# Kernel tuning notes

Measured on AMD Instinct MI355X. Metric: run time of the kernel, lower is better.

The kernel has to match this reference:

```python
import jax, jax.numpy as jnp
import numpy as np

B, C, H, Wd = 4, 64, 64, 64


def setup_inputs() -> dict:
    key = jax.random.key(0)
    k1, k2, k3 = jax.random.split(key, 3)
    x = jax.random.normal(k1, (B, C, H, Wd), dtype=jnp.float32)
    W = jax.random.normal(k2, (C, C), dtype=jnp.float32) * (1.0 / np.sqrt(C))
    b = jax.random.normal(k3, (C,), dtype=jnp.float32) * 0.01
    return {"x": x, "W": W, "b": b}


def reference(x, W, b):
    Bz, Cz, Hz, Wz = x.shape
    N = Hz * Wz
    xf = x.reshape(Bz, Cz, N)                      # values [B,C,N]
    # shared 1x1 conv for queries and keys (same module instance in torch)
    qk = jnp.einsum('oc,bcn->bon', W, xf) + b[None, :, None]  # [B,C,N]
    # scores[b,n,m] = sum_c q[b,c,n] * k[b,c,m], scaled by 1/N
    scores = jnp.einsum('bcn,bcm->bnm', qk, qk) / N           # [B,N,N]
    attn = jax.nn.softmax(scores, axis=-1)                    # softmax over m
    # out[b,c,n] = sum_m values[b,c,m] * attn[b,n,m]
    out = jnp.einsum('bcm,bnm->bcn', xf, attn)
    return out.reshape(Bz, Cz, Hz, Wz)
```

## Files before the change

kernel.cpp:

```cpp
#include <hip/hip_runtime.h>
#include <hip/hip_bf16.h>

#define BATCH 4
#define NSP   4096

typedef __bf16 bf16x8v __attribute__((ext_vector_type(8)));
typedef __bf16 bf16x4v __attribute__((ext_vector_type(4)));
typedef float  floatx4 __attribute__((ext_vector_type(4)));

__global__ __launch_bounds__(256) void qk_kernel(const float* __restrict__ x,
                                                 const float* __restrict__ Wm,
                                                 const float* __restrict__ bias,
                                                 __bf16* __restrict__ qkT) {
    __shared__ __align__(16) char smem1[18432];
    __bf16* xT   = (__bf16*)smem1;
    __bf16* Wl   = (__bf16*)(smem1 + 9216);
    float*  Olds = (float*)smem1;

    const int t  = threadIdx.x;
    const int b  = blockIdx.x >> 6;
    const int n0 = (blockIdx.x & 63) << 6;

#pragma unroll
    for (int i = 0; i < 16; ++i) {
        int idx = t + 256 * i;
        int r = idx >> 6, j = idx & 63;
        xT[j * 72 + r] = (__bf16)x[(b * 64 + r) * 4096 + n0 + j];
        Wl[r * 72 + j] = (__bf16)Wm[idx];
    }
    __syncthreads();

    const int w = t >> 6, lane = t & 63, quad = lane >> 4, l16 = lane & 15;
    const bf16x8v a0 = *(const bf16x8v*)(xT + (w * 16 + l16) * 72 + quad * 8);
    const bf16x8v a1 = *(const bf16x8v*)(xT + (w * 16 + l16) * 72 + 32 + quad * 8);

    floatx4 acc[4];
#pragma unroll
    for (int ot = 0; ot < 4; ++ot) {
        acc[ot] = floatx4{0.f, 0.f, 0.f, 0.f};
        bf16x8v b0 = *(const bf16x8v*)(Wl + (ot * 16 + l16) * 72 + quad * 8);
        bf16x8v b1 = *(const bf16x8v*)(Wl + (ot * 16 + l16) * 72 + 32 + quad * 8);
        acc[ot] = __builtin_amdgcn_mfma_f32_16x16x32_bf16(a0, b0, acc[ot], 0, 0, 0);
        acc[ot] = __builtin_amdgcn_mfma_f32_16x16x32_bf16(a1, b1, acc[ot], 0, 0, 0);
    }
    __syncthreads();

#pragma unroll
    for (int ot = 0; ot < 4; ++ot) {
        const float bo = bias[ot * 16 + l16];
#pragma unroll
        for (int r = 0; r < 4; ++r)
            Olds[(w * 16 + quad * 4 + r) * 68 + ot * 16 + l16] = acc[ot][r] + bo;
    }
    __syncthreads();

    const int n = t >> 2, seg = t & 3;
#pragma unroll
    for (int i = 0; i < 2; ++i) {
        bf16x8v pk;
#pragma unroll
        for (int k = 0; k < 8; ++k)
            pk[k] = (__bf16)Olds[n * 68 + seg * 16 + i * 8 + k];
        *(bf16x8v*)(qkT + (size_t)(b * 4096 + n0 + n) * 64 + seg * 16 + i * 8) = pk;
    }
}

#define KSTRIDE 72
#define OSTRIDE 68

__global__ __launch_bounds__(256, 4) void attn_kernel(const float* __restrict__ x,
                                                      const __bf16* __restrict__ qkT,
                                                      __bf16* __restrict__ Opart,
                                                      float* __restrict__ Lpart) {
    __shared__ __align__(16) char smem[27648];
    __bf16* Klds = (__bf16*)smem;
    __bf16* Vlds = (__bf16*)(smem + 9216);
    __bf16* Plds = (__bf16*)(smem + 18432);
    float*  Olds = (float*)smem;

    const int t   = threadIdx.x;
    const int blk = blockIdx.x;
    const int xcd = blk & 7;
    const int b   = xcd >> 1;
    const int sub = ((blk >> 3) << 1) | (xcd & 1);
    const int qt  = sub >> 2;
    const int s   = sub & 3;
    const int n0  = qt << 6;
    const int pblk = (b * 64 + qt) * 4 + s;

    const int w = t >> 6, lane = t & 63, quad = lane >> 4, l16 = lane & 15;

    const __bf16* qrow = qkT + (size_t)(b * 4096 + n0 + w * 16 + l16) * 64;
    const bf16x8v fq0 = *(const bf16x8v*)(qrow + quad * 8);
    const bf16x8v fq1 = *(const bf16x8v*)(qrow + 32 + quad * 8);

    floatx4 o0 = {0.f, 0.f, 0.f, 0.f};
    floatx4 o1 = {0.f, 0.f, 0.f, 0.f};
    floatx4 o2 = {0.f, 0.f, 0.f, 0.f};
    floatx4 o3 = {0.f, 0.f, 0.f, 0.f};
    float rs[4] = {0.f, 0.f, 0.f, 0.f};
    const float scale = 1.0f / 4096.0f;

    for (int it = 0; it < 16; ++it) {
        const int m0 = (s << 10) + (it << 6);
        __syncthreads();
#pragma unroll
        for (int i = 0; i < 2; ++i) {
            int idx = t + 256 * i;
            int row = idx >> 3, c8 = idx & 7;
            *(uint4*)(Klds + row * KSTRIDE + c8 * 8) =
                *(const uint4*)(qkT + (size_t)(b * 4096 + m0 + row) * 64 + c8 * 8);
        }
#pragma unroll
        for (int i = 0; i < 4; ++i) {
            int idx = t + 256 * i;
            int c = idx >> 4, f4 = idx & 15;
            const float4 v = *(const float4*)(x + (size_t)(b * 64 + c) * 4096 + m0 + f4 * 4);
            bf16x4v bv;
            bv[0] = (__bf16)v.x; bv[1] = (__bf16)v.y; bv[2] = (__bf16)v.z; bv[3] = (__bf16)v.w;
            *(bf16x4v*)(Vlds + c * KSTRIDE + f4 * 4) = bv;
        }
        __syncthreads();

#pragma unroll
        for (int mt = 0; mt < 4; ++mt) {
            const __bf16* kr = Klds + (mt * 16 + l16) * KSTRIDE;
            bf16x8v bk0 = *(const bf16x8v*)(kr + quad * 8);
            bf16x8v bk1 = *(const bf16x8v*)(kr + 32 + quad * 8);
            floatx4 sA = {0.f, 0.f, 0.f, 0.f};
            sA = __builtin_amdgcn_mfma_f32_16x16x32_bf16(fq0, bk0, sA, 0, 0, 0);
            sA = __builtin_amdgcn_mfma_f32_16x16x32_bf16(fq1, bk1, sA, 0, 0, 0);
#pragma unroll
            for (int r = 0; r < 4; ++r) {
                float p = __expf(sA[r] * scale);
                rs[r] += p;
                Plds[(w * 16 + quad * 4 + r) * KSTRIDE + mt * 16 + l16] = (__bf16)p;
            }
        }

        const __bf16* pr = Plds + (w * 16 + l16) * KSTRIDE;
        bf16x8v ap0 = *(const bf16x8v*)(pr + quad * 8);
        bf16x8v ap1 = *(const bf16x8v*)(pr + 32 + quad * 8);
        {
            const __bf16* vr0 = Vlds + (0 * 16 + l16) * KSTRIDE;
            const __bf16* vr1 = Vlds + (1 * 16 + l16) * KSTRIDE;
            const __bf16* vr2 = Vlds + (2 * 16 + l16) * KSTRIDE;
            const __bf16* vr3 = Vlds + (3 * 16 + l16) * KSTRIDE;
            o0 = __builtin_amdgcn_mfma_f32_16x16x32_bf16(ap0, *(const bf16x8v*)(vr0 + quad * 8), o0, 0, 0, 0);
            o0 = __builtin_amdgcn_mfma_f32_16x16x32_bf16(ap1, *(const bf16x8v*)(vr0 + 32 + quad * 8), o0, 0, 0, 0);
            o1 = __builtin_amdgcn_mfma_f32_16x16x32_bf16(ap0, *(const bf16x8v*)(vr1 + quad * 8), o1, 0, 0, 0);
            o1 = __builtin_amdgcn_mfma_f32_16x16x32_bf16(ap1, *(const bf16x8v*)(vr1 + 32 + quad * 8), o1, 0, 0, 0);
            o2 = __builtin_amdgcn_mfma_f32_16x16x32_bf16(ap0, *(const bf16x8v*)(vr2 + quad * 8), o2, 0, 0, 0);
            o2 = __builtin_amdgcn_mfma_f32_16x16x32_bf16(ap1, *(const bf16x8v*)(vr2 + 32 + quad * 8), o2, 0, 0, 0);
            o3 = __builtin_amdgcn_mfma_f32_16x16x32_bf16(ap0, *(const bf16x8v*)(vr3 + quad * 8), o3, 0, 0, 0);
            o3 = __builtin_amdgcn_mfma_f32_16x16x32_bf16(ap1, *(const bf16x8v*)(vr3 + 32 + quad * 8), o3, 0, 0, 0);
        }
    }

#pragma unroll
    for (int r = 0; r < 4; ++r) {
        float v = rs[r];
        v += __shfl_xor(v, 1, 64);
        v += __shfl_xor(v, 2, 64);
        v += __shfl_xor(v, 4, 64);
        v += __shfl_xor(v, 8, 64);
        if (l16 == 0)
            Lpart[(size_t)pblk * 64 + w * 16 + quad * 4 + r] = v;
    }

    __syncthreads();

    floatx4 oo[4] = {o0, o1, o2, o3};
#pragma unroll
    for (int ct = 0; ct < 4; ++ct)
#pragma unroll
        for (int r = 0; r < 4; ++r)
            Olds[(ct * 16 + l16) * OSTRIDE + (w * 16 + quad * 4 + r)] = oo[ct][r];
    __syncthreads();

    const int c = t >> 2, seg = t & 3;
    const size_t obase = (size_t)pblk * 4096 + c * 64 + seg * 16;
#pragma unroll
    for (int i = 0; i < 2; ++i) {
        bf16x8v pk;
#pragma unroll
        for (int k = 0; k < 8; ++k)
            pk[k] = (__bf16)Olds[c * OSTRIDE + seg * 16 + i * 8 + k];
        *(bf16x8v*)(Opart + obase + i * 8) = pk;
    }
}

__global__ __launch_bounds__(256) void reduce_kernel(const __bf16* __restrict__ Opart,
                                                     const float* __restrict__ Lpart,
                                                     float* __restrict__ out) {
    __shared__ float linv[64];
    const int blk = blockIdx.x;
    const int b = blk >> 6, qt = blk & 63;
    const int t = threadIdx.x;

    if (t < 64) {
        float sl = 0.f;
#pragma unroll
        for (int ss = 0; ss < 4; ++ss)
            sl += Lpart[((size_t)blk * 4 + ss) * 64 + t];
        linv[t] = 1.0f / sl;
    }
    __syncthreads();

    const int c = t >> 2, seg = t & 3;
    float acc[16];
#pragma unroll
    for (int k = 0; k < 16; ++k) acc[k] = 0.f;
#pragma unroll
    for (int ss = 0; ss < 4; ++ss) {
        const __bf16* p = Opart + ((size_t)blk * 4 + ss) * 4096 + c * 64 + seg * 16;
        bf16x8v v0 = *(const bf16x8v*)p;
        bf16x8v v1 = *(const bf16x8v*)(p + 8);
#pragma unroll
        for (int k = 0; k < 8; ++k) { acc[k] += (float)v0[k]; acc[8 + k] += (float)v1[k]; }
    }
    float* op = out + (size_t)(b * 64 + c) * 4096 + qt * 64 + seg * 16;
#pragma unroll
    for (int k = 0; k < 16; ++k) acc[k] *= linv[seg * 16 + k];
#pragma unroll
    for (int i = 0; i < 4; ++i) {
        float4 vv = {acc[i * 4], acc[i * 4 + 1], acc[i * 4 + 2], acc[i * 4 + 3]};
        *(float4*)(op + i * 4) = vv;
    }
}

extern "C" void kernel_launch(void* const* d_in, const int* in_sizes, int n_in,
                              void* d_out, int out_size, void* d_ws, size_t ws_size,
                              hipStream_t stream) {
    const float* x    = (const float*)d_in[0];
    const float* Wm   = (const float*)d_in[1];
    const float* bias = (const float*)d_in[2];
    float* out = (float*)d_out;

    char* ws = (char*)d_ws;
    __bf16* qkT   = (__bf16*)ws;
    __bf16* Opart = (__bf16*)(ws + 2097152);
    float*  Lpart = (float*)(ws + 2097152 + 8388608);

    qk_kernel<<<BATCH * (NSP / 64), 256, 0, stream>>>(x, Wm, bias, qkT);
    attn_kernel<<<BATCH * 64 * 4, 256, 0, stream>>>(x, qkT, Opart, Lpart);
    reduce_kernel<<<BATCH * 64, 256, 0, stream>>>(Opart, Lpart, out);
}
```

Before: 111.0 us.

## Use 128-query attention tiles with 8-way key split and folded score scaling

Each attention block now handles 128 queries (two 16-row tiles per wave), so every K/V tile staged in LDS feeds twice as many MFMAs and global K/V traffic per query drops. The key range is split eight ways when the workspace allows it, to keep the grid size up. The 1/N score scale is folded into q/k by multiplying x and bias by 1/64 in the qk kernel, which removes the per-element multiply before exp. The qk kernel shrinks to 64-thread blocks that read W directly from global memory, and the reduce kernel is rebalanced to match. The cost is more registers and LDS per block, which may lower occupancy, plus bf16 rounding of the pre-scaled q/k values.

```diff
diff --git a/kernel.cpp b/kernel.cpp
--- a/kernel.cpp
+++ b/kernel.cpp
@@ -8,38 +8,42 @@
 typedef __bf16 bf16x4v __attribute__((ext_vector_type(4)));
 typedef float  floatx4 __attribute__((ext_vector_type(4)));
 
-__global__ __launch_bounds__(256) void qk_kernel(const float* __restrict__ x,
-                                                 const float* __restrict__ Wm,
-                                                 const float* __restrict__ bias,
-                                                 __bf16* __restrict__ qkT) {
-    __shared__ __align__(16) char smem1[18432];
-    __bf16* xT   = (__bf16*)smem1;
-    __bf16* Wl   = (__bf16*)(smem1 + 9216);
-    float*  Olds = (float*)smem1;
+__global__ __launch_bounds__(64) void qk_kernel(const float* __restrict__ x,
+                                                const float* __restrict__ Wm,
+                                                const float* __restrict__ bias,
+                                                __bf16* __restrict__ qkT) {
+    __shared__ __align__(16) __bf16 xT[16 * 72];
 
     const int t  = threadIdx.x;
-    const int b  = blockIdx.x >> 6;
-    const int n0 = (blockIdx.x & 63) << 6;
+    const int b  = blockIdx.x >> 8;
+    const int n0 = (blockIdx.x & 255) << 4;
 
 #pragma unroll
     for (int i = 0; i < 16; ++i) {
-        int idx = t + 256 * i;
-        int r = idx >> 6, j = idx & 63;
-        xT[j * 72 + r] = (__bf16)x[(b * 64 + r) * 4096 + n0 + j];
-        Wl[r * 72 + j] = (__bf16)Wm[idx];
-    }
-    __syncthreads();
-
-    const int w = t >> 6, lane = t & 63, quad = lane >> 4, l16 = lane & 15;
-    const bf16x8v a0 = *(const bf16x8v*)(xT + (w * 16 + l16) * 72 + quad * 8);
-    const bf16x8v a1 = *(const bf16x8v*)(xT + (w * 16 + l16) * 72 + 32 + quad * 8);
+        int idx = t + 64 * i;
+        int c = idx >> 4, n = idx & 15;
+        xT[n * 72 + c] = (__bf16)(x[(size_t)(b * 64 + c) * 4096 + n0 + n] * 0.015625f);
+    }
+    __syncthreads();
+
+    const int quad = t >> 4, l16 = t & 15;
+    const bf16x8v a0 = *(const bf16x8v*)(xT + l16 * 72 + quad * 8);
+    const bf16x8v a1 = *(const bf16x8v*)(xT + l16 * 72 + 32 + quad * 8);
 
     floatx4 acc[4];
 #pragma unroll
     for (int ot = 0; ot < 4; ++ot) {
+        const float* wr = Wm + (ot * 16 + l16) * 64;
+        float4 wa = *(const float4*)(wr + quad * 8);
+        float4 wb = *(const float4*)(wr + quad * 8 + 4);
+        float4 wc = *(const float4*)(wr + 32 + quad * 8);
+        float4 wd = *(const float4*)(wr + 32 + quad * 8 + 4);
+        bf16x8v b0, b1;
+        b0[0]=(__bf16)wa.x; b0[1]=(__bf16)wa.y; b0[2]=(__bf16)wa.z; b0[3]=(__bf16)wa.w;
+        b0[4]=(__bf16)wb.x; b0[5]=(__bf16)wb.y; b0[6]=(__bf16)wb.z; b0[7]=(__bf16)wb.w;
+        b1[0]=(__bf16)wc.x; b1[1]=(__bf16)wc.y; b1[2]=(__bf16)wc.z; b1[3]=(__bf16)wc.w;
+        b1[4]=(__bf16)wd.x; b1[5]=(__bf16)wd.y; b1[6]=(__bf16)wd.z; b1[7]=(__bf16)wd.w;
         acc[ot] = floatx4{0.f, 0.f, 0.f, 0.f};
-        bf16x8v b0 = *(const bf16x8v*)(Wl + (ot * 16 + l16) * 72 + quad * 8);
-        bf16x8v b1 = *(const bf16x8v*)(Wl + (ot * 16 + l16) * 72 + 32 + quad * 8);
         acc[ot] = __builtin_amdgcn_mfma_f32_16x16x32_bf16(a0, b0, acc[ot], 0, 0, 0);
         acc[ot] = __builtin_amdgcn_mfma_f32_16x16x32_bf16(a1, b1, acc[ot], 0, 0, 0);
     }
@@ -47,32 +51,25 @@
 
 #pragma unroll
     for (int ot = 0; ot < 4; ++ot) {
-        const float bo = bias[ot * 16 + l16];
+        const float bo = bias[ot * 16 + l16] * 0.015625f;
 #pragma unroll
         for (int r = 0; r < 4; ++r)
-            Olds[(w * 16 + quad * 4 + r) * 68 + ot * 16 + l16] = acc[ot][r] + bo;
+            xT[(quad * 4 + r) * 72 + ot * 16 + l16] = (__bf16)(acc[ot][r] + bo);
     }
     __syncthreads();
 
     const int n = t >> 2, seg = t & 3;
-#pragma unroll
-    for (int i = 0; i < 2; ++i) {
-        bf16x8v pk;
-#pragma unroll
-        for (int k = 0; k < 8; ++k)
-            pk[k] = (__bf16)Olds[n * 68 + seg * 16 + i * 8 + k];
-        *(bf16x8v*)(qkT + (size_t)(b * 4096 + n0 + n) * 64 + seg * 16 + i * 8) = pk;
-    }
-}
-
-#define KSTRIDE 72
-#define OSTRIDE 68
-
+    __bf16* dst = qkT + (size_t)(b * 4096 + n0 + n) * 64 + seg * 16;
+    *(bf16x8v*)dst       = *(const bf16x8v*)(xT + n * 72 + seg * 16);
+    *(bf16x8v*)(dst + 8) = *(const bf16x8v*)(xT + n * 72 + seg * 16 + 8);
+}
+
+template<int SPLIT, int ITERS>
 __global__ __launch_bounds__(256, 4) void attn_kernel(const float* __restrict__ x,
                                                       const __bf16* __restrict__ qkT,
                                                       __bf16* __restrict__ Opart,
                                                       float* __restrict__ Lpart) {
-    __shared__ __align__(16) char smem[27648];
+    __shared__ __align__(16) char smem[36864];
     __bf16* Klds = (__bf16*)smem;
     __bf16* Vlds = (__bf16*)(smem + 9216);
     __bf16* Plds = (__bf16*)(smem + 18432);
@@ -83,32 +80,36 @@
     const int xcd = blk & 7;
     const int b   = xcd >> 1;
     const int sub = ((blk >> 3) << 1) | (xcd & 1);
-    const int qt  = sub >> 2;
-    const int s   = sub & 3;
-    const int n0  = qt << 6;
-    const int pblk = (b * 64 + qt) * 4 + s;
+    const int qt  = sub / SPLIT;
+    const int s   = sub % SPLIT;
+    const int n0  = qt << 7;
+    const int pblk = (b * 32 + qt) * SPLIT + s;
 
     const int w = t >> 6, lane = t & 63, quad = lane >> 4, l16 = lane & 15;
 
-    const __bf16* qrow = qkT + (size_t)(b * 4096 + n0 + w * 16 + l16) * 64;
-    const bf16x8v fq0 = *(const bf16x8v*)(qrow + quad * 8);
-    const bf16x8v fq1 = *(const bf16x8v*)(qrow + 32 + quad * 8);
-
-    floatx4 o0 = {0.f, 0.f, 0.f, 0.f};
-    floatx4 o1 = {0.f, 0.f, 0.f, 0.f};
-    floatx4 o2 = {0.f, 0.f, 0.f, 0.f};
-    floatx4 o3 = {0.f, 0.f, 0.f, 0.f};
-    float rs[4] = {0.f, 0.f, 0.f, 0.f};
-    const float scale = 1.0f / 4096.0f;
-
-    for (int it = 0; it < 16; ++it) {
-        const int m0 = (s << 10) + (it << 6);
+    bf16x8v fq[2][2];
+#pragma unroll
+    for (int qt2 = 0; qt2 < 2; ++qt2) {
+        const __bf16* qrow = qkT + (size_t)(b * 4096 + n0 + w * 32 + qt2 * 16 + l16) * 64;
+        fq[qt2][0] = *(const bf16x8v*)(qrow + quad * 8);
+        fq[qt2][1] = *(const bf16x8v*)(qrow + 32 + quad * 8);
+    }
+
+    floatx4 oacc[2][4];
+#pragma unroll
+    for (int i = 0; i < 2; ++i)
+#pragma unroll
+        for (int j = 0; j < 4; ++j) oacc[i][j] = floatx4{0.f, 0.f, 0.f, 0.f};
+    float rs[2] = {0.f, 0.f};
+
+    for (int it = 0; it < ITERS; ++it) {
+        const int m0 = s * (64 * ITERS) + (it << 6);
         __syncthreads();
 #pragma unroll
         for (int i = 0; i < 2; ++i) {
             int idx = t + 256 * i;
             int row = idx >> 3, c8 = idx & 7;
-            *(uint4*)(Klds + row * KSTRIDE + c8 * 8) =
+            *(uint4*)(Klds + row * 72 + c8 * 8) =
                 *(const uint4*)(qkT + (size_t)(b * 4096 + m0 + row) * 64 + c8 * 8);
         }
 #pragma unroll
@@ -118,115 +119,108 @@
             const float4 v = *(const float4*)(x + (size_t)(b * 64 + c) * 4096 + m0 + f4 * 4);
             bf16x4v bv;
             bv[0] = (__bf16)v.x; bv[1] = (__bf16)v.y; bv[2] = (__bf16)v.z; bv[3] = (__bf16)v.w;
-            *(bf16x4v*)(Vlds + c * KSTRIDE + f4 * 4) = bv;
+            *(bf16x4v*)(Vlds + c * 72 + f4 * 4) = bv;
         }
         __syncthreads();
 
 #pragma unroll
         for (int mt = 0; mt < 4; ++mt) {
-            const __bf16* kr = Klds + (mt * 16 + l16) * KSTRIDE;
-            bf16x8v bk0 = *(const bf16x8v*)(kr + quad * 8);
-            bf16x8v bk1 = *(const bf16x8v*)(kr + 32 + quad * 8);
-            floatx4 sA = {0.f, 0.f, 0.f, 0.f};
-            sA = __builtin_amdgcn_mfma_f32_16x16x32_bf16(fq0, bk0, sA, 0, 0, 0);
-            sA = __builtin_amdgcn_mfma_f32_16x16x32_bf16(fq1, bk1, sA, 0, 0, 0);
-#pragma unroll
-            for (int r = 0; r < 4; ++r) {
-                float p = __expf(sA[r] * scale);
-                rs[r] += p;
-                Plds[(w * 16 + quad * 4 + r) * KSTRIDE + mt * 16 + l16] = (__bf16)p;
+            const __bf16* kr = Klds + (mt * 16 + l16) * 72;
+            bf16x8v ak0 = *(const bf16x8v*)(kr + quad * 8);
+            bf16x8v ak1 = *(const bf16x8v*)(kr + 32 + quad * 8);
+#pragma unroll
+            for (int qt2 = 0; qt2 < 2; ++qt2) {
+                floatx4 sT = {0.f, 0.f, 0.f, 0.f};
+                sT = __builtin_amdgcn_mfma_f32_16x16x32_bf16(ak0, fq[qt2][0], sT, 0, 0, 0);
+                sT = __builtin_amdgcn_mfma_f32_16x16x32_bf16(ak1, fq[qt2][1], sT, 0, 0, 0);
+                float p0 = __expf(sT[0]), p1 = __expf(sT[1]);
+                float p2 = __expf(sT[2]), p3 = __expf(sT[3]);
+                rs[qt2] += (p0 + p1) + (p2 + p3);
+                bf16x4v pv;
+                pv[0] = (__bf16)p0; pv[1] = (__bf16)p1; pv[2] = (__bf16)p2; pv[3] = (__bf16)p3;
+                *(bf16x4v*)(Plds + (w * 32 + qt2 * 16 + l16) * 72 + mt * 16 + quad * 4) = pv;
             }
         }
 
-        const __bf16* pr = Plds + (w * 16 + l16) * KSTRIDE;
-        bf16x8v ap0 = *(const bf16x8v*)(pr + quad * 8);
-        bf16x8v ap1 = *(const bf16x8v*)(pr + 32 + quad * 8);
-        {
-            const __bf16* vr0 = Vlds + (0 * 16 + l16) * KSTRIDE;
-            const __bf16* vr1 = Vlds + (1 * 16 + l16) * KSTRIDE;
-            const __bf16* vr2 = Vlds + (2 * 16 + l16) * KSTRIDE;
-            const __bf16* vr3 = Vlds + (3 * 16 + l16) * KSTRIDE;
-            o0 = __builtin_amdgcn_mfma_f32_16x16x32_bf16(ap0, *(const bf16x8v*)(vr0 + quad * 8), o0, 0, 0, 0);
-            o0 = __builtin_amdgcn_mfma_f32_16x16x32_bf16(ap1, *(const bf16x8v*)(vr0 + 32 + quad * 8), o0, 0, 0, 0);
-            o1 = __builtin_amdgcn_mfma_f32_16x16x32_bf16(ap0, *(const bf16x8v*)(vr1 + quad * 8), o1, 0, 0, 0);
-            o1 = __builtin_amdgcn_mfma_f32_16x16x32_bf16(ap1, *(const bf16x8v*)(vr1 + 32 + quad * 8), o1, 0, 0, 0);
-            o2 = __builtin_amdgcn_mfma_f32_16x16x32_bf16(ap0, *(const bf16x8v*)(vr2 + quad * 8), o2, 0, 0, 0);
-            o2 = __builtin_amdgcn_mfma_f32_16x16x32_bf16(ap1, *(const bf16x8v*)(vr2 + 32 + quad * 8), o2, 0, 0, 0);
-            o3 = __builtin_amdgcn_mfma_f32_16x16x32_bf16(ap0, *(const bf16x8v*)(vr3 + quad * 8), o3, 0, 0, 0);
-            o3 = __builtin_amdgcn_mfma_f32_16x16x32_bf16(ap1, *(const bf16x8v*)(vr3 + 32 + quad * 8), o3, 0, 0, 0);
-        }
-    }
-
-#pragma unroll
-    for (int r = 0; r < 4; ++r) {
-        float v = rs[r];
-        v += __shfl_xor(v, 1, 64);
-        v += __shfl_xor(v, 2, 64);
-        v += __shfl_xor(v, 4, 64);
-        v += __shfl_xor(v, 8, 64);
-        if (l16 == 0)
-            Lpart[(size_t)pblk * 64 + w * 16 + quad * 4 + r] = v;
-    }
-
-    __syncthreads();
-
-    floatx4 oo[4] = {o0, o1, o2, o3};
-#pragma unroll
-    for (int ct = 0; ct < 4; ++ct)
-#pragma unroll
-        for (int r = 0; r < 4; ++r)
-            Olds[(ct * 16 + l16) * OSTRIDE + (w * 16 + quad * 4 + r)] = oo[ct][r];
+        bf16x8v ap[2][2];
+#pragma unroll
+        for (int qt2 = 0; qt2 < 2; ++qt2) {
+            const __bf16* pr = Plds + (w * 32 + qt2 * 16 + l16) * 72;
+            ap[qt2][0] = *(const bf16x8v*)(pr + quad * 8);
+            ap[qt2][1] = *(const bf16x8v*)(pr + 32 + quad * 8);
+        }
+#pragma unroll
+        for (int ct = 0; ct < 4; ++ct) {
+            const __bf16* vr = Vlds + (ct * 16 + l16) * 72;
+            bf16x8v bv0 = *(const bf16x8v*)(vr + quad * 8);
+            bf16x8v bv1 = *(const bf16x8v*)(vr + 32 + quad * 8);
+#pragma unroll
+            for (int qt2 = 0; qt2 < 2; ++qt2) {
+                oacc[qt2][ct] = __builtin_amdgcn_mfma_f32_16x16x32_bf16(ap[qt2][0], bv0, oacc[qt2][ct], 0, 0, 0);
+                oacc[qt2][ct] = __builtin_amdgcn_mfma_f32_16x16x32_bf16(ap[qt2][1], bv1, oacc[qt2][ct], 0, 0, 0);
+            }
+        }
+    }
+
+#pragma unroll
+    for (int qt2 = 0; qt2 < 2; ++qt2) {
+        float v = rs[qt2];
+        v += __shfl_xor(v, 16, 64);
+        v += __shfl_xor(v, 32, 64);
+        if (quad == 0)
+            Lpart[(size_t)pblk * 128 + w * 32 + qt2 * 16 + l16] = v;
+    }
+
+    __syncthreads();
+
+#pragma unroll
+    for (int qt2 = 0; qt2 < 2; ++qt2)
+#pragma unroll
+        for (int ct = 0; ct < 4; ++ct)
+#pragma unroll
+            for (int r = 0; r < 4; ++r)
+                Olds[(ct * 16 + l16) * 132 + w * 32 + qt2 * 16 + quad * 4 + r] = oacc[qt2][ct][r];
     __syncthreads();
 
     const int c = t >> 2, seg = t & 3;
-    const size_t obase = (size_t)pblk * 4096 + c * 64 + seg * 16;
-#pragma unroll
-    for (int i = 0; i < 2; ++i) {
+#pragma unroll
+    for (int i = 0; i < 4; ++i) {
+        floatx4 v0 = *(const floatx4*)(Olds + c * 132 + seg * 32 + i * 8);
+        floatx4 v1 = *(const floatx4*)(Olds + c * 132 + seg * 32 + i * 8 + 4);
         bf16x8v pk;
-#pragma unroll
-        for (int k = 0; k < 8; ++k)
-            pk[k] = (__bf16)Olds[c * OSTRIDE + seg * 16 + i * 8 + k];
-        *(bf16x8v*)(Opart + obase + i * 8) = pk;
-    }
-}
-
+        pk[0]=(__bf16)v0[0]; pk[1]=(__bf16)v0[1]; pk[2]=(__bf16)v0[2]; pk[3]=(__bf16)v0[3];
+        pk[4]=(__bf16)v1[0]; pk[5]=(__bf16)v1[1]; pk[6]=(__bf16)v1[2]; pk[7]=(__bf16)v1[3];
+        *(bf16x8v*)(Opart + (size_t)pblk * 8192 + c * 128 + seg * 32 + i * 8) = pk;
+    }
+}
+
+template<int SPLIT>
 __global__ __launch_bounds__(256) void reduce_kernel(const __bf16* __restrict__ Opart,
                                                      const float* __restrict__ Lpart,
                                                      float* __restrict__ out) {
-    __shared__ float linv[64];
     const int blk = blockIdx.x;
-    const int b = blk >> 6, qt = blk & 63;
+    const int bq = blk >> 3, cq = blk & 7;
+    const int b = bq >> 5, qt = bq & 31;
     const int t = threadIdx.x;
-
-    if (t < 64) {
-        float sl = 0.f;
-#pragma unroll
-        for (int ss = 0; ss < 4; ++ss)
-            sl += Lpart[((size_t)blk * 4 + ss) * 64 + t];
-        linv[t] = 1.0f / sl;
-    }
-    __syncthreads();
-
-    const int c = t >> 2, seg = t & 3;
-    float acc[16];
-#pragma unroll
-    for (int k = 0; k < 16; ++k) acc[k] = 0.f;
-#pragma unroll
-    for (int ss = 0; ss < 4; ++ss) {
-        const __bf16* p = Opart + ((size_t)blk * 4 + ss) * 4096 + c * 64 + seg * 16;
-        bf16x8v v0 = *(const bf16x8v*)p;
-        bf16x8v v1 = *(const bf16x8v*)(p + 8);
-#pragma unroll
-        for (int k = 0; k < 8; ++k) { acc[k] += (float)v0[k]; acc[8 + k] += (float)v1[k]; }
-    }
-    float* op = out + (size_t)(b * 64 + c) * 4096 + qt * 64 + seg * 16;
-#pragma unroll
-    for (int k = 0; k < 16; ++k) acc[k] *= linv[seg * 16 + k];
-#pragma unroll
-    for (int i = 0; i < 4; ++i) {
-        float4 vv = {acc[i * 4], acc[i * 4 + 1], acc[i * 4 + 2], acc[i * 4 + 3]};
-        *(float4*)(op + i * 4) = vv;
-    }
+    const int cl = t >> 5;
+    const int q4 = (t & 31) << 2;
+
+    float l0 = 0.f, l1 = 0.f, l2 = 0.f, l3 = 0.f;
+#pragma unroll
+    for (int s = 0; s < SPLIT; ++s) {
+        const float4 lv = *(const float4*)(Lpart + ((size_t)bq * SPLIT + s) * 128 + q4);
+        l0 += lv.x; l1 += lv.y; l2 += lv.z; l3 += lv.w;
+    }
+    float a0 = 0.f, a1 = 0.f, a2 = 0.f, a3 = 0.f;
+#pragma unroll
+    for (int s = 0; s < SPLIT; ++s) {
+        const __bf16* p = Opart + ((size_t)bq * SPLIT + s) * 8192 + (cq * 8 + cl) * 128 + q4;
+        bf16x4v v = *(const bf16x4v*)p;
+        a0 += (float)v[0]; a1 += (float)v[1]; a2 += (float)v[2]; a3 += (float)v[3];
+    }
+    float4 o;
+    o.x = a0 / l0; o.y = a1 / l1; o.z = a2 / l2; o.w = a3 / l3;
+    *(float4*)(out + (size_t)(b * 64 + cq * 8 + cl) * 4096 + qt * 128 + q4) = o;
 }
 
 extern "C" void kernel_launch(void* const* d_in, const int* in_sizes, int n_in,
@@ -238,11 +232,21 @@
     float* out = (float*)d_out;
 
     char* ws = (char*)d_ws;
-    __bf16* qkT   = (__bf16*)ws;
-    __bf16* Opart = (__bf16*)(ws + 2097152);
-    float*  Lpart = (float*)(ws + 2097152 + 8388608);
-
-    qk_kernel<<<BATCH * (NSP / 64), 256, 0, stream>>>(x, Wm, bias, qkT);
-    attn_kernel<<<BATCH * 64 * 4, 256, 0, stream>>>(x, qkT, Opart, Lpart);
-    reduce_kernel<<<BATCH * 64, 256, 0, stream>>>(Opart, Lpart, out);
-}
+    __bf16* qkT = (__bf16*)ws;
+
+    qk_kernel<<<BATCH * (NSP / 16), 64, 0, stream>>>(x, Wm, bias, qkT);
+
+    const size_t QKT = 2097152;
+    const size_t needBig = QKT + (size_t)1024 * 8192 * 2 + (size_t)1024 * 128 * 4;
+    if (ws_size >= needBig) {
+        __bf16* Opart = (__bf16*)(ws + QKT);
+        float*  Lpart = (float*)(ws + QKT + (size_t)1024 * 8192 * 2);
+        attn_kernel<8, 8><<<BATCH * 32 * 8, 256, 0, stream>>>(x, qkT, Opart, Lpart);
+        reduce_kernel<8><<<1024, 256, 0, stream>>>(Opart, Lpart, out);
+    } else {
+        __bf16* Opart = (__bf16*)(ws + QKT);
+        float*  Lpart = (float*)(ws + QKT + (size_t)512 * 8192 * 2);
+        attn_kernel<4, 16><<<BATCH * 32 * 4, 256, 0, stream>>>(x, qkT, Opart, Lpart);
+        reduce_kernel<4><<<1024, 256, 0, stream>>>(Opart, Lpart, out);
+    }
+}
```

Result: faster. 101.8 us (-8.3%).
